# Kernel optimization log

Hardware: AMD Instinct MI355X
Metric: run time of the kernel (lower is better)

Reference implementation:

```python
import jax, jax.numpy as jnp
import numpy as np

FP8_E4M3_MAX = 448.0  # max representable magnitude of float8_e4m3fn

def fake_quant_fp8(t):
    """Per-tensor dynamic-scale fp8 (e4m3) quantize + dequantize."""
    amax = jnp.max(jnp.abs(t))
    scale = FP8_E4M3_MAX / jnp.maximum(amax, 1e-12)
    q = (t * scale).astype(jnp.float8_e4m3fn).astype(jnp.float32)
    return q / scale

def setup_inputs() -> dict:
    key = jax.random.key(0)
    k1, k2, k3 = jax.random.split(key, 3)
    d_in, d_out = 1024, 1024
    x = jax.random.normal(k1, (4, 8192, d_in), dtype=jnp.float32)
    weight = jax.random.normal(k2, (d_out, d_in), dtype=jnp.float32) * (1.0 / np.sqrt(d_in))
    bias = jax.random.normal(k3, (d_out,), dtype=jnp.float32) * 0.01
    return {"x": x, "weight": weight, "bias": bias}

def reference(x, weight, bias):
    # fp8-quantized linear: quantize activations and weights to e4m3 with
    # per-tensor dynamic scales, matmul, dequant (folded into fake-quant), add bias.
    xq = fake_quant_fp8(x)        # [b, s, d_in]
    wq = fake_quant_fp8(weight)   # [d_out, d_in]
    return jnp.einsum('bsd,od->bso', xq, wq) + bias
```

## Files before the change

kernel.cpp:

```cpp
#include <hip/hip_runtime.h>
#include <stdint.h>

typedef float floatx4 __attribute__((ext_vector_type(4)));
typedef int intx8 __attribute__((ext_vector_type(8)));

#define FP8_MAX 448.0f
#define BM 128
#define BN 128
#define BK 128
#define GX 2048
#define GW 256

__global__ void amax_partial(const float* __restrict__ x, long n4x,
                             const float* __restrict__ w, long n4w,
                             float* __restrict__ part) {
    const float4* p4; long n4, i0, stride;
    if (blockIdx.x < GX) {
        p4 = (const float4*)x; n4 = n4x;
        i0 = (long)blockIdx.x * blockDim.x + threadIdx.x;
        stride = (long)GX * blockDim.x;
    } else {
        p4 = (const float4*)w; n4 = n4w;
        i0 = (long)(blockIdx.x - GX) * blockDim.x + threadIdx.x;
        stride = (long)GW * blockDim.x;
    }
    float m = 0.f;
    for (long i = i0; i < n4; i += stride) {
        float4 v = p4[i];
        m = fmaxf(m, fmaxf(fmaxf(fabsf(v.x), fabsf(v.y)),
                           fmaxf(fabsf(v.z), fabsf(v.w))));
    }
    #pragma unroll
    for (int off = 32; off > 0; off >>= 1) m = fmaxf(m, __shfl_down(m, off, 64));
    __shared__ float red[4];
    if ((threadIdx.x & 63) == 0) red[threadIdx.x >> 6] = m;
    __syncthreads();
    if (threadIdx.x == 0)
        part[blockIdx.x] = fmaxf(fmaxf(red[0], red[1]), fmaxf(red[2], red[3]));
}

__global__ void finalize_scales(const float* __restrict__ part, float* __restrict__ scales) {
    float mx = 0.f, mw = 0.f;
    for (int i = threadIdx.x; i < GX; i += 256) mx = fmaxf(mx, part[i]);
    for (int i = GX + threadIdx.x; i < GX + GW; i += 256) mw = fmaxf(mw, part[i]);
    #pragma unroll
    for (int off = 32; off > 0; off >>= 1) {
        mx = fmaxf(mx, __shfl_down(mx, off, 64));
        mw = fmaxf(mw, __shfl_down(mw, off, 64));
    }
    __shared__ float rx[4], rw[4];
    if ((threadIdx.x & 63) == 0) { rx[threadIdx.x >> 6] = mx; rw[threadIdx.x >> 6] = mw; }
    __syncthreads();
    if (threadIdx.x == 0) {
        float ax = fmaxf(fmaxf(rx[0], rx[1]), fmaxf(rx[2], rx[3]));
        float aw = fmaxf(fmaxf(rw[0], rw[1]), fmaxf(rw[2], rw[3]));
        float sx = FP8_MAX / fmaxf(ax, 1e-12f);
        float sw = FP8_MAX / fmaxf(aw, 1e-12f);
        scales[0] = sx; scales[1] = sw; scales[2] = 1.0f / (sx * sw);
    }
}

__global__ void quant_kernel(const float* __restrict__ x, int4* __restrict__ xq, long n16x,
                             const float* __restrict__ w, int4* __restrict__ wq, long n16w,
                             const float* __restrict__ scales) {
    const float4* p4; int4* o; long n16, i0, stride; float s;
    if (blockIdx.x < GX) {
        p4 = (const float4*)x; o = xq; n16 = n16x; s = scales[0];
        i0 = (long)blockIdx.x * blockDim.x + threadIdx.x;
        stride = (long)GX * blockDim.x;
    } else {
        p4 = (const float4*)w; o = wq; n16 = n16w; s = scales[1];
        i0 = (long)(blockIdx.x - GX) * blockDim.x + threadIdx.x;
        stride = (long)GW * blockDim.x;
    }
    for (long i = i0; i < n16; i += stride) {
        float4 v0 = p4[i * 4 + 0];
        float4 v1 = p4[i * 4 + 1];
        float4 v2 = p4[i * 4 + 2];
        float4 v3 = p4[i * 4 + 3];
        int w0 = 0, w1 = 0, w2 = 0, w3 = 0;
        w0 = __builtin_amdgcn_cvt_pk_fp8_f32(v0.x * s, v0.y * s, w0, false);
        w0 = __builtin_amdgcn_cvt_pk_fp8_f32(v0.z * s, v0.w * s, w0, true);
        w1 = __builtin_amdgcn_cvt_pk_fp8_f32(v1.x * s, v1.y * s, w1, false);
        w1 = __builtin_amdgcn_cvt_pk_fp8_f32(v1.z * s, v1.w * s, w1, true);
        w2 = __builtin_amdgcn_cvt_pk_fp8_f32(v2.x * s, v2.y * s, w2, false);
        w2 = __builtin_amdgcn_cvt_pk_fp8_f32(v2.z * s, v2.w * s, w2, true);
        w3 = __builtin_amdgcn_cvt_pk_fp8_f32(v3.x * s, v3.y * s, w3, false);
        w3 = __builtin_amdgcn_cvt_pk_fp8_f32(v3.z * s, v3.w * s, w3, true);
        o[i] = make_int4(w0, w1, w2, w3);
    }
}

__global__ __launch_bounds__(256) void gemm_fp8mx(
    const unsigned char* __restrict__ Aq, const unsigned char* __restrict__ Bq,
    const float* __restrict__ bias, const float* __restrict__ scales,
    float* __restrict__ out, int M, int N, int K) {
    __shared__ __align__(16) unsigned char tA[BM * BK];
    __shared__ __align__(16) unsigned char tB[BN * BK];

    const int tid = threadIdx.x;
    const int lane = tid & 63;
    const int wave = tid >> 6;
    const int waveM = (wave & 1) * 64;
    const int waveN = (wave >> 1) * 64;

    const int nbx = gridDim.x;
    const int nwg = nbx * gridDim.y;
    int bx = blockIdx.x, by = blockIdx.y;
    if (nbx == 8 && (nwg & 7) == 0) {
        const int f   = by * 8 + bx;
        const int per = nwg >> 3;
        const int sw  = (f & 7) * per + (f >> 3);
        bx = sw & 7;
        by = sw >> 3;
    }
    const long m0 = (long)by * BM;
    const int n0 = bx * BN;

    const int srow = lane >> 3;
    const int sphys = lane & 7;

    floatx4 acc[4][4];
    #pragma unroll
    for (int i = 0; i < 4; ++i)
        #pragma unroll
        for (int j = 0; j < 4; ++j)
            acc[i][j] = (floatx4){0.f, 0.f, 0.f, 0.f};

    const int row16 = lane & 15;
    const int q2 = (lane >> 4) * 2;

    for (int k0 = 0; k0 < K; k0 += BK) {
        __syncthreads();
        #pragma unroll
        for (int c = 0; c < 4; ++c) {
            const int r = wave * 32 + c * 8 + srow;
            const int lc = (sphys ^ (r & 7)) * 16;
            __builtin_amdgcn_global_load_lds(
                (const __attribute__((address_space(1))) void*)(Aq + (m0 + r) * (long)K + k0 + lc),
                (__attribute__((address_space(3))) void*)&tA[r * BK + sphys * 16], 16, 0, 0);
            __builtin_amdgcn_global_load_lds(
                (const __attribute__((address_space(1))) void*)(Bq + (long)(n0 + r) * K + k0 + lc),
                (__attribute__((address_space(3))) void*)&tB[r * BK + sphys * 16], 16, 0, 0);
        }
        __syncthreads();

        intx8 af[4], bf[4];
        #pragma unroll
        for (int t = 0; t < 4; ++t) {
            const int row = waveM + t * 16 + row16;
            const int s = row & 7;
            const int4 lo = *(const int4*)&tA[row * BK + ((q2 ^ s)) * 16];
            const int4 hi = *(const int4*)&tA[row * BK + (((q2 + 1) ^ s)) * 16];
            af[t] = (intx8){lo.x, lo.y, lo.z, lo.w, hi.x, hi.y, hi.z, hi.w};
        }
        #pragma unroll
        for (int t = 0; t < 4; ++t) {
            const int row = waveN + t * 16 + row16;
            const int s = row & 7;
            const int4 lo = *(const int4*)&tB[row * BK + ((q2 ^ s)) * 16];
            const int4 hi = *(const int4*)&tB[row * BK + (((q2 + 1) ^ s)) * 16];
            bf[t] = (intx8){lo.x, lo.y, lo.z, lo.w, hi.x, hi.y, hi.z, hi.w};
        }
        #pragma unroll
        for (int mt = 0; mt < 4; ++mt)
            #pragma unroll
            for (int nt = 0; nt < 4; ++nt)
                acc[mt][nt] = __builtin_amdgcn_mfma_scale_f32_16x16x128_f8f6f4(
                    af[mt], bf[nt], acc[mt][nt], 0, 0,
                    0, 127, 0, 127);
    }

    const float inv = scales[2];
    const int col = lane & 15;
    const int rbase4 = (lane >> 4) * 4;
    #pragma unroll
    for (int nt = 0; nt < 4; ++nt) {
        const int gn = n0 + waveN + nt * 16 + col;
        const float bv = bias[gn];
        #pragma unroll
        for (int mt = 0; mt < 4; ++mt) {
            const long gm = m0 + waveM + mt * 16 + rbase4;
            float* po = out + gm * (long)N + gn;
            #pragma unroll
            for (int r = 0; r < 4; ++r)
                po[(long)r * N] = acc[mt][nt][r] * inv + bv;
        }
    }
}

extern "C" void kernel_launch(void* const* d_in, const int* in_sizes, int n_in,
                              void* d_out, int out_size, void* d_ws, size_t ws_size,
                              hipStream_t stream) {
    const float* x = (const float*)d_in[0];
    const float* w = (const float*)d_in[1];
    const float* bias = (const float*)d_in[2];
    float* out = (float*)d_out;

    const long nx = in_sizes[0];
    const long nw = in_sizes[1];
    const int N = in_sizes[2];
    const long K = nw / N;
    const long M = nx / K;

    unsigned char* ws = (unsigned char*)d_ws;
    unsigned char* xq = ws;
    unsigned char* wq = ws + nx;
    float* part = (float*)(ws + nx + nw);
    float* scales = (float*)(ws + nx + nw + 16384);

    amax_partial<<<GX + GW, 256, 0, stream>>>(x, nx / 4, w, nw / 4, part);
    finalize_scales<<<1, 256, 0, stream>>>(part, scales);
    quant_kernel<<<GX + GW, 256, 0, stream>>>(x, (int4*)xq, nx / 16,
                                              w, (int4*)wq, nw / 16, scales);

    dim3 grid(N / BN, (int)(M / BM));
    gemm_fp8mx<<<grid, 256, 0, stream>>>(xq, wq, bias, scales, out,
                                         (int)M, N, (int)K);
}
```

Before: 297.3 us.

## Fuse activation fp8 quantization into GEMM tile loads and merge weight quant with scales

Removes the standalone quantization pass over activations; the GEMM now loads fp32 activations, scales and converts them to fp8 in registers, and stores them into the swizzled LDS tile. Weight quantization is merged with scale finalization into one kernel, with each block recomputing the scales. This avoids writing and re-reading the quantized activation buffer and drops one launch. In exchange, each column-tile block rereads fp32 activations and redoes the conversion, and the A-tile load becomes synchronous through registers instead of direct-to-LDS.

```diff
diff --git a/kernel.cpp b/kernel.cpp
--- a/kernel.cpp
+++ b/kernel.cpp
@@ -39,60 +39,50 @@
         part[blockIdx.x] = fmaxf(fmaxf(red[0], red[1]), fmaxf(red[2], red[3]));
 }
 
-__global__ void finalize_scales(const float* __restrict__ part, float* __restrict__ scales) {
+__global__ void quantw_scales(const float* __restrict__ part,
+                              const float* __restrict__ w, int4* __restrict__ wq,
+                              long n16w, float* __restrict__ scales) {
+    const int tid = threadIdx.x;
     float mx = 0.f, mw = 0.f;
-    for (int i = threadIdx.x; i < GX; i += 256) mx = fmaxf(mx, part[i]);
-    for (int i = GX + threadIdx.x; i < GX + GW; i += 256) mw = fmaxf(mw, part[i]);
+    for (int i = tid; i < GX; i += 256) mx = fmaxf(mx, part[i]);
+    for (int i = GX + tid; i < GX + GW; i += 256) mw = fmaxf(mw, part[i]);
     #pragma unroll
     for (int off = 32; off > 0; off >>= 1) {
         mx = fmaxf(mx, __shfl_down(mx, off, 64));
         mw = fmaxf(mw, __shfl_down(mw, off, 64));
     }
     __shared__ float rx[4], rw[4];
-    if ((threadIdx.x & 63) == 0) { rx[threadIdx.x >> 6] = mx; rw[threadIdx.x >> 6] = mw; }
+    if ((tid & 63) == 0) { rx[tid >> 6] = mx; rw[tid >> 6] = mw; }
     __syncthreads();
-    if (threadIdx.x == 0) {
-        float ax = fmaxf(fmaxf(rx[0], rx[1]), fmaxf(rx[2], rx[3]));
-        float aw = fmaxf(fmaxf(rw[0], rw[1]), fmaxf(rw[2], rw[3]));
-        float sx = FP8_MAX / fmaxf(ax, 1e-12f);
-        float sw = FP8_MAX / fmaxf(aw, 1e-12f);
+    const float ax = fmaxf(fmaxf(rx[0], rx[1]), fmaxf(rx[2], rx[3]));
+    const float aw = fmaxf(fmaxf(rw[0], rw[1]), fmaxf(rw[2], rw[3]));
+    const float sx = FP8_MAX / fmaxf(ax, 1e-12f);
+    const float sw = FP8_MAX / fmaxf(aw, 1e-12f);
+    if (blockIdx.x == 0 && tid == 0) {
         scales[0] = sx; scales[1] = sw; scales[2] = 1.0f / (sx * sw);
     }
-}
-
-__global__ void quant_kernel(const float* __restrict__ x, int4* __restrict__ xq, long n16x,
-                             const float* __restrict__ w, int4* __restrict__ wq, long n16w,
-                             const float* __restrict__ scales) {
-    const float4* p4; int4* o; long n16, i0, stride; float s;
-    if (blockIdx.x < GX) {
-        p4 = (const float4*)x; o = xq; n16 = n16x; s = scales[0];
-        i0 = (long)blockIdx.x * blockDim.x + threadIdx.x;
-        stride = (long)GX * blockDim.x;
-    } else {
-        p4 = (const float4*)w; o = wq; n16 = n16w; s = scales[1];
-        i0 = (long)(blockIdx.x - GX) * blockDim.x + threadIdx.x;
-        stride = (long)GW * blockDim.x;
-    }
-    for (long i = i0; i < n16; i += stride) {
+    const float4* p4 = (const float4*)w;
+    const long i = (long)blockIdx.x * 256 + tid;
+    if (i < n16w) {
         float4 v0 = p4[i * 4 + 0];
         float4 v1 = p4[i * 4 + 1];
         float4 v2 = p4[i * 4 + 2];
         float4 v3 = p4[i * 4 + 3];
         int w0 = 0, w1 = 0, w2 = 0, w3 = 0;
-        w0 = __builtin_amdgcn_cvt_pk_fp8_f32(v0.x * s, v0.y * s, w0, false);
-        w0 = __builtin_amdgcn_cvt_pk_fp8_f32(v0.z * s, v0.w * s, w0, true);
-        w1 = __builtin_amdgcn_cvt_pk_fp8_f32(v1.x * s, v1.y * s, w1, false);
-        w1 = __builtin_amdgcn_cvt_pk_fp8_f32(v1.z * s, v1.w * s, w1, true);
-        w2 = __builtin_amdgcn_cvt_pk_fp8_f32(v2.x * s, v2.y * s, w2, false);
-        w2 = __builtin_amdgcn_cvt_pk_fp8_f32(v2.z * s, v2.w * s, w2, true);
-        w3 = __builtin_amdgcn_cvt_pk_fp8_f32(v3.x * s, v3.y * s, w3, false);
-        w3 = __builtin_amdgcn_cvt_pk_fp8_f32(v3.z * s, v3.w * s, w3, true);
-        o[i] = make_int4(w0, w1, w2, w3);
+        w0 = __builtin_amdgcn_cvt_pk_fp8_f32(v0.x * sw, v0.y * sw, w0, false);
+        w0 = __builtin_amdgcn_cvt_pk_fp8_f32(v0.z * sw, v0.w * sw, w0, true);
+        w1 = __builtin_amdgcn_cvt_pk_fp8_f32(v1.x * sw, v1.y * sw, w1, false);
+        w1 = __builtin_amdgcn_cvt_pk_fp8_f32(v1.z * sw, v1.w * sw, w1, true);
+        w2 = __builtin_amdgcn_cvt_pk_fp8_f32(v2.x * sw, v2.y * sw, w2, false);
+        w2 = __builtin_amdgcn_cvt_pk_fp8_f32(v2.z * sw, v2.w * sw, w2, true);
+        w3 = __builtin_amdgcn_cvt_pk_fp8_f32(v3.x * sw, v3.y * sw, w3, false);
+        w3 = __builtin_amdgcn_cvt_pk_fp8_f32(v3.z * sw, v3.w * sw, w3, true);
+        wq[i] = make_int4(w0, w1, w2, w3);
     }
 }
 
 __global__ __launch_bounds__(256) void gemm_fp8mx(
-    const unsigned char* __restrict__ Aq, const unsigned char* __restrict__ Bq,
+    const float* __restrict__ xf, const unsigned char* __restrict__ Bq,
     const float* __restrict__ bias, const float* __restrict__ scales,
     float* __restrict__ out, int M, int N, int K) {
     __shared__ __align__(16) unsigned char tA[BM * BK];
@@ -120,6 +110,9 @@
     const int srow = lane >> 3;
     const int sphys = lane & 7;
 
+    const float sx = scales[0];
+    const float inv = scales[2];
+
     floatx4 acc[4][4];
     #pragma unroll
     for (int i = 0; i < 4; ++i)
@@ -129,6 +122,9 @@
 
     const int row16 = lane & 15;
     const int q2 = (lane >> 4) * 2;
+
+    const float4* x4 = (const float4*)xf;
+    const int K4 = K >> 2;
 
     for (int k0 = 0; k0 < K; k0 += BK) {
         __syncthreads();
@@ -137,11 +133,30 @@
             const int r = wave * 32 + c * 8 + srow;
             const int lc = (sphys ^ (r & 7)) * 16;
             __builtin_amdgcn_global_load_lds(
-                (const __attribute__((address_space(1))) void*)(Aq + (m0 + r) * (long)K + k0 + lc),
-                (__attribute__((address_space(3))) void*)&tA[r * BK + sphys * 16], 16, 0, 0);
-            __builtin_amdgcn_global_load_lds(
                 (const __attribute__((address_space(1))) void*)(Bq + (long)(n0 + r) * K + k0 + lc),
                 (__attribute__((address_space(3))) void*)&tB[r * BK + sphys * 16], 16, 0, 0);
+        }
+        #pragma unroll
+        for (int j = 0; j < 4; ++j) {
+            const int fidx = (tid << 2) + (j << 10);
+            const int row = fidx >> 5;
+            const int c4 = fidx & 31;
+            const float4* px = x4 + (m0 + row) * (long)K4 + (k0 >> 2) + c4;
+            const float4 v0 = px[0];
+            const float4 v1 = px[1];
+            const float4 v2 = px[2];
+            const float4 v3 = px[3];
+            int w0 = 0, w1 = 0, w2 = 0, w3 = 0;
+            w0 = __builtin_amdgcn_cvt_pk_fp8_f32(v0.x * sx, v0.y * sx, w0, false);
+            w0 = __builtin_amdgcn_cvt_pk_fp8_f32(v0.z * sx, v0.w * sx, w0, true);
+            w1 = __builtin_amdgcn_cvt_pk_fp8_f32(v1.x * sx, v1.y * sx, w1, false);
+            w1 = __builtin_amdgcn_cvt_pk_fp8_f32(v1.z * sx, v1.w * sx, w1, true);
+            w2 = __builtin_amdgcn_cvt_pk_fp8_f32(v2.x * sx, v2.y * sx, w2, false);
+            w2 = __builtin_amdgcn_cvt_pk_fp8_f32(v2.z * sx, v2.w * sx, w2, true);
+            w3 = __builtin_amdgcn_cvt_pk_fp8_f32(v3.x * sx, v3.y * sx, w3, false);
+            w3 = __builtin_amdgcn_cvt_pk_fp8_f32(v3.z * sx, v3.w * sx, w3, true);
+            const int phys = (tid & 7) ^ (row & 7);
+            *(int4*)&tA[row * BK + phys * 16] = make_int4(w0, w1, w2, w3);
         }
         __syncthreads();
 
@@ -171,7 +186,6 @@
                     0, 127, 0, 127);
     }
 
-    const float inv = scales[2];
     const int col = lane & 15;
     const int rbase4 = (lane >> 4) * 4;
     #pragma unroll
@@ -204,17 +218,14 @@
     const long M = nx / K;
 
     unsigned char* ws = (unsigned char*)d_ws;
-    unsigned char* xq = ws;
-    unsigned char* wq = ws + nx;
-    float* part = (float*)(ws + nx + nw);
-    float* scales = (float*)(ws + nx + nw + 16384);
+    unsigned char* wq = ws;
+    float* part = (float*)(ws + nw);
+    float* scales = (float*)(ws + nw + 16384);
 
     amax_partial<<<GX + GW, 256, 0, stream>>>(x, nx / 4, w, nw / 4, part);
-    finalize_scales<<<1, 256, 0, stream>>>(part, scales);
-    quant_kernel<<<GX + GW, 256, 0, stream>>>(x, (int4*)xq, nx / 16,
-                                              w, (int4*)wq, nw / 16, scales);
+    quantw_scales<<<GW, 256, 0, stream>>>(part, w, (int4*)wq, nw / 16, scales);
 
     dim3 grid(N / BN, (int)(M / BM));
-    gemm_fp8mx<<<grid, 256, 0, stream>>>(xq, wq, bias, scales, out,
+    gemm_fp8mx<<<grid, 256, 0, stream>>>(x, wq, bias, scales, out,
                                          (int)M, N, (int)K);
 }
```

Result: slower. 314.9 us (+5.9%).
